# Optimization experiments

Hardware: AMD Instinct MI355X
Metric: run time of the kernel (lower is better)

The kernel has to match this reference:

```python
import jax, jax.numpy as jnp
import numpy as np

HEADS = 4


def setup_inputs() -> dict:
    key = jax.random.key(0)
    kx, kqkv, kbq, ko, kbo = jax.random.split(key, 5)
    B, C, H, W = 4, 256, 64, 64
    x = jax.random.normal(kx, (B, C, H, W), dtype=jnp.float32)
    # torch nn.Linear stores weight as [out_features, in_features]
    w_qkv = jax.random.normal(kqkv, (3 * C, C), dtype=jnp.float32) * (1.0 / np.sqrt(C))
    b_qkv = jax.random.normal(kbq, (3 * C,), dtype=jnp.float32) * 0.02
    w_o = jax.random.normal(ko, (C, C), dtype=jnp.float32) * (1.0 / np.sqrt(C))
    b_o = jax.random.normal(kbo, (C,), dtype=jnp.float32) * 0.02
    return {"x": x, "w_qkv": w_qkv, "b_qkv": b_qkv, "w_o": w_o, "b_o": b_o}


def reference(x, w_qkv, b_qkv, w_o, b_o):
    B, C, H, W = x.shape
    S = H * W
    hd = C // HEADS
    # (B, C, H, W) -> (B, S, C)
    xt = x.reshape(B, C, S).transpose(0, 2, 1)
    qkv = xt @ w_qkv.T + b_qkv                      # (B, S, 3C)
    q, k, v = jnp.split(qkv, 3, axis=-1)
    def to_heads(t):
        return t.reshape(B, S, HEADS, hd).transpose(0, 2, 1, 3)  # (B, h, S, hd)
    q, k, v = to_heads(q), to_heads(k), to_heads(v)
    scores = jnp.einsum('bhqd,bhkd->bhqk', q, k) / jnp.sqrt(jnp.float32(hd))
    attn = jax.nn.softmax(scores, axis=-1)          # dropout inactive (eval)
    out = jnp.einsum('bhqk,bhkd->bhqd', attn, v)    # (B, h, S, hd)
    out = out.transpose(0, 2, 1, 3).reshape(B, S, C)
    y = out @ w_o.T + b_o                            # (B, S, C)
    y = y.reshape(B, H, W, C).transpose(0, 3, 1, 2)  # (B, C, H, W)
    return y
```

## Files before the change

kernel.cpp:

```cpp
#include <hip/hip_runtime.h>
#include <stdint.h>

#define DI __device__ __forceinline__

typedef __attribute__((ext_vector_type(8))) __bf16 bf16x8;
typedef __attribute__((ext_vector_type(8))) unsigned short u16x8;
typedef __attribute__((ext_vector_type(4))) float f32x4;
typedef __attribute__((ext_vector_type(4))) uint32_t u32x4;
typedef __attribute__((ext_vector_type(4))) unsigned short u16x4;
typedef unsigned short u16;

constexpr int Bb = 4, Cc = 256, Ss = 4096, HD = 64;
constexpr int ELEMS = Bb * Cc * Ss;

DI u16 f2bf(float f) {
  union { float f; unsigned u; } x; x.f = f;
  return (u16)((x.u + 0x7FFFu + ((x.u >> 16) & 1u)) >> 16);
}
DI uint32_t pack2bf(float a, float b) {
  union { float f; uint32_t u; } xa, xb;
  xa.f = a; xb.f = b;
  return __builtin_amdgcn_perm(xb.u + 0x8000u, xa.u + 0x8000u, 0x07060302u);
}
DI bf16x8 ldfrag(const u16* p) { return __builtin_bit_cast(bf16x8, *(const u16x8*)p); }

__global__ __launch_bounds__(256) void k_convw(const float* __restrict__ w1, const float* __restrict__ w2,
                                               u16* __restrict__ d1, u16* __restrict__ d2) {
  int i = blockIdx.x * 256 + threadIdx.x;
  if (i < 196608) d1[i] = f2bf(w1[i]);
  if (i < 65536) d2[i] = f2bf(w2[i]);
}

__global__ __launch_bounds__(256) void k_transpose(const float* __restrict__ x, u16* __restrict__ xt) {
  __shared__ u16 T[64][72];
  const int st = blockIdx.x, ct = blockIdx.y, b = blockIdx.z;
  const int tid = threadIdx.x;
#pragma unroll
  for (int e = 0; e < 2; e++) {
    int ss = tid + e * 256;
    int r = ss >> 3, seg = ss & 7;
    size_t base = ((size_t)(b * Cc + ct * 64 + r) << 12) + st * 64 + seg * 8;
    u16x8 t;
#pragma unroll
    for (int j = 0; j < 8; j++) t[j] = f2bf(x[base + j]);
    *(u16x8*)&T[r][seg * 8] = t;
  }
  __syncthreads();
#pragma unroll
  for (int e = 0; e < 2; e++) {
    int ss = tid + e * 256;
    int sr = ss >> 3, cseg = ss & 7;
    u16x8 o;
#pragma unroll
    for (int j = 0; j < 8; j++) o[j] = T[cseg * 8 + j][sr];
    *(u16x8*)(xt + ((size_t)(b * Ss + st * 64 + sr) << 8) + ct * 64 + cseg * 8) = o;
  }
}

DI void stage_tile(const u16* __restrict__ src, int pitch, int r0, int k0, u16 (*dst)[40], int tid) {
#pragma unroll
  for (int e = 0; e < 2; e++) {
    int c = tid + e * 256;
    int row = c >> 2, seg = c & 3;
    u16x8 t = *(const u16x8*)(src + (size_t)(r0 + row) * pitch + k0 + seg * 8);
    *(u16x8*)&dst[row][seg * 8] = t;
  }
}

__global__ __launch_bounds__(256) void k_qkv(const u16* __restrict__ xt, const u16* __restrict__ w,
                                             const float* __restrict__ bias,
                                             u16* __restrict__ q, u16* __restrict__ kk_, u16* __restrict__ vt_) {
  __shared__ u16 As[128][40], Bs[128][40];
  const int tid = threadIdx.x;
  const int wv = tid >> 6, lane = tid & 63;
  const int wm = wv >> 1, wn = wv & 1;
  const int lr = lane & 15, quad = lane >> 4;
  const int r0 = blockIdx.x * 128;
  const int j0 = blockIdx.y * 128;
  f32x4 acc[4][4] = {};
  for (int k0 = 0; k0 < 256; k0 += 32) {
    __syncthreads();
    stage_tile(xt, 256, r0, k0, As, tid);
    stage_tile(w, 256, j0, k0, Bs, tid);
    __syncthreads();
    bf16x8 a[4], b[4];
#pragma unroll
    for (int mt = 0; mt < 4; mt++) a[mt] = ldfrag(&As[wm * 64 + mt * 16 + lr][quad * 8]);
#pragma unroll
    for (int nt = 0; nt < 4; nt++) b[nt] = ldfrag(&Bs[wn * 64 + nt * 16 + lr][quad * 8]);
#pragma unroll
    for (int mt = 0; mt < 4; mt++)
#pragma unroll
      for (int nt = 0; nt < 4; nt++)
        acc[mt][nt] = __builtin_amdgcn_mfma_f32_16x16x32_bf16(a[mt], b[nt], acc[mt][nt], 0, 0, 0);
  }
#pragma unroll
  for (int nt = 0; nt < 4; nt++) {
    int j = j0 + wn * 64 + nt * 16 + lr;
    float bj = bias[j];
    int part = j >> 8, cc = j & 255, head = cc >> 6, d = cc & 63;
#pragma unroll
    for (int mt = 0; mt < 4; mt++)
#pragma unroll
      for (int rg = 0; rg < 4; rg++) {
        int row = r0 + wm * 64 + mt * 16 + quad * 4 + rg;
        int b_ = row >> 12, s = row & 4095;
        float val = acc[mt][nt][rg] + bj;
        if (part == 0) {
          q[((size_t)((b_ * 4 + head) * Ss + s) << 6) + d] = f2bf(val * 0.18033688f);
        } else if (part == 1) {
          kk_[((size_t)((b_ * 4 + head) * Ss + s) << 6) + d] = f2bf(val);
        } else {
          int chunk = s >> 6, w6 = s & 63;
          int t = w6 >> 4, qq = (w6 >> 2) & 3, r = w6 & 3;
          int slot = ((t >> 1) << 5) | (qq << 3) | ((t & 1) << 2) | r;
          vt_[((size_t)((b_ * 4 + head) * 64 + d) << 12) + chunk * 64 + slot] = f2bf(val);
        }
      }
  }
}

__global__ __launch_bounds__(256, 2) void k_attn(const u16* __restrict__ Q, const u16* __restrict__ K,
                                                 const u16* __restrict__ VT, u16* __restrict__ AO,
                                                 float* __restrict__ Opart, float* __restrict__ lpart,
                                                 int nsplit) {
  __shared__ u16 Kl[2][64][72];
  __shared__ u16 Vl[2][64][72];
  const int tid = threadIdx.x;
  const int wv = tid >> 6, lane = tid & 63;
  const int lr = lane & 15, quad = lane >> 4;
  const int bh = blockIdx.y;
  const int b_ = bh >> 2, head = bh & 3;
  const int qbase = blockIdx.x * 256 + wv * 64;
  const int sp = blockIdx.z;
  const int nchunk = 64 / nsplit, kcg0 = sp * nchunk;
  const u16* Qh = Q + (size_t)bh * Ss * HD;
  const u16* Kh = K + (size_t)bh * Ss * HD;
  const u16* Vh = VT + (size_t)bh * HD * Ss;

  bf16x8 qb[4][2];
#pragma unroll
  for (int nt = 0; nt < 4; nt++)
#pragma unroll
    for (int ks = 0; ks < 2; ks++)
      qb[nt][ks] = ldfrag(Qh + (size_t)(qbase + nt * 16 + lr) * HD + ks * 32 + quad * 8);

  f32x4 O[4][4] = {};
  float lsum[4] = {0.f, 0.f, 0.f, 0.f};

  u16x8 pf[4];
  const int srow = tid >> 3, sseg = tid & 7;
  auto load_chunk = [&](int kc) {
#pragma unroll
    for (int e = 0; e < 2; e++) {
      pf[e] = *(const u16x8*)(Kh + ((size_t)((kcg0 + kc) * 64 + srow + e * 32) << 6) + sseg * 8);
      pf[2 + e] = *(const u16x8*)(Vh + ((size_t)(srow + e * 32) << 12) + (kcg0 + kc) * 64 + sseg * 8);
    }
  };
  auto store_chunk = [&](int buf) {
#pragma unroll
    for (int e = 0; e < 2; e++) {
      *(u16x8*)&Kl[buf][srow + e * 32][sseg * 8] = pf[e];
      *(u16x8*)&Vl[buf][srow + e * 32][sseg * 8] = pf[2 + e];
    }
  };

  load_chunk(0);
  store_chunk(0);
  if (nchunk > 1) load_chunk(1);
  __syncthreads();

  for (int kc = 0; kc < nchunk; kc++) {
    const int cur = kc & 1;
    f32x4 St[4][4] = {};
#pragma unroll
    for (int ks = 0; ks < 2; ks++) {
      bf16x8 ka[4];
#pragma unroll
      for (int kt = 0; kt < 4; kt++) ka[kt] = ldfrag(&Kl[cur][kt * 16 + lr][ks * 32 + quad * 8]);
#pragma unroll
      for (int kt = 0; kt < 4; kt++)
#pragma unroll
        for (int nt = 0; nt < 4; nt++)
          St[kt][nt] = __builtin_amdgcn_mfma_f32_16x16x32_bf16(ka[kt], qb[nt][ks], St[kt][nt], 0, 0, 0);
    }

    uint32_t pk[4][4][2];
#pragma unroll
    for (int kt = 0; kt < 4; kt++)
#pragma unroll
      for (int nt = 0; nt < 4; nt++) {
        float p0 = __builtin_amdgcn_exp2f(St[kt][nt][0]);
        float p1 = __builtin_amdgcn_exp2f(St[kt][nt][1]);
        float p2 = __builtin_amdgcn_exp2f(St[kt][nt][2]);
        float p3 = __builtin_amdgcn_exp2f(St[kt][nt][3]);
        lsum[nt] += (p0 + p1) + (p2 + p3);
        pk[kt][nt][0] = pack2bf(p0, p1);
        pk[kt][nt][1] = pack2bf(p2, p3);
      }

#pragma unroll
    for (int ks = 0; ks < 2; ks++) {
      bf16x8 pa[4];
#pragma unroll
      for (int mt = 0; mt < 4; mt++) {
        u32x4 t = {pk[2 * ks][mt][0], pk[2 * ks][mt][1], pk[2 * ks + 1][mt][0], pk[2 * ks + 1][mt][1]};
        pa[mt] = __builtin_bit_cast(bf16x8, t);
      }
#pragma unroll
      for (int dt = 0; dt < 4; dt++) {
        bf16x8 vb = ldfrag(&Vl[cur][dt * 16 + lr][ks * 32 + quad * 8]);
#pragma unroll
        for (int mt = 0; mt < 4; mt++)
          O[mt][dt] = __builtin_amdgcn_mfma_f32_16x16x32_bf16(pa[mt], vb, O[mt][dt], 0, 0, 0);
      }
    }

    if (kc + 1 < nchunk) {
      store_chunk(cur ^ 1);
      if (kc + 2 < nchunk) load_chunk(kc + 2);
    }
    __syncthreads();
  }

#pragma unroll
  for (int nt = 0; nt < 4; nt++) {
    lsum[nt] += __shfl_xor(lsum[nt], 16);
    lsum[nt] += __shfl_xor(lsum[nt], 32);
  }

  if (nsplit == 1) {
#pragma unroll
    for (int mt = 0; mt < 4; mt++)
#pragma unroll
      for (int rg = 0; rg < 4; rg++) {
        float lv = __shfl(lsum[mt], quad * 4 + rg + (lane & 48));
        lv = __shfl(lsum[mt], quad * 4 + rg);
        float inv = 1.0f / lv;
        int s = qbase + mt * 16 + quad * 4 + rg;
#pragma unroll
        for (int dt = 0; dt < 4; dt++)
          AO[((size_t)(b_ * Ss + s) << 8) + head * 64 + dt * 16 + lr] = f2bf(O[mt][dt][rg] * inv);
      }
  } else {
    float* Op = Opart + (size_t)sp * ELEMS;
    float* lp = lpart + (size_t)sp * (16 * Ss) + bh * Ss;
    if (quad == 0) {
#pragma unroll
      for (int nt = 0; nt < 4; nt++) lp[qbase + nt * 16 + lr] = lsum[nt];
    }
#pragma unroll
    for (int mt = 0; mt < 4; mt++)
#pragma unroll
      for (int rg = 0; rg < 4; rg++) {
        int s = qbase + mt * 16 + quad * 4 + rg;
#pragma unroll
        for (int dt = 0; dt < 4; dt++)
          Op[((size_t)(b_ * Ss + s) << 8) + head * 64 + dt * 16 + lr] = O[mt][dt][rg];
      }
  }
}

__global__ __launch_bounds__(256) void k_comb(const float* __restrict__ Opart, const float* __restrict__ lpart,
                                              u16* __restrict__ ao) {
  int idx = (blockIdx.x * 256 + threadIdx.x) * 4;
  f32x4 o0 = *(const f32x4*)(Opart + idx);
  f32x4 o1 = *(const f32x4*)(Opart + (size_t)ELEMS + idx);
  int c = idx & 255, bs = idx >> 8;
  int b = bs >> 12, s = bs & 4095, head = c >> 6;
  int li = (b * 4 + head) * Ss + s;
  float l = lpart[li] + lpart[16 * Ss + li];
  float inv = 1.0f / l;
  u16x4 o;
#pragma unroll
  for (int j = 0; j < 4; j++) o[j] = f2bf((o0[j] + o1[j]) * inv);
  *(u16x4*)(ao + idx) = o;
}

__global__ __launch_bounds__(256) void k_oproj(const u16* __restrict__ wo, const u16* __restrict__ ao,
                                               const float* __restrict__ bo, float* __restrict__ y) {
  __shared__ u16 As[128][40], Bs[128][40];
  const int tid = threadIdx.x;
  const int wv = tid >> 6, lane = tid & 63;
  const int wm = wv >> 1, wn = wv & 1;
  const int lr = lane & 15, quad = lane >> 4;
  const int c0 = blockIdx.x * 128;
  const int n0 = blockIdx.y * 128;
  f32x4 acc[4][4] = {};
  for (int k0 = 0; k0 < 256; k0 += 32) {
    __syncthreads();
    stage_tile(wo, 256, c0, k0, As, tid);
    stage_tile(ao, 256, n0, k0, Bs, tid);
    __syncthreads();
    bf16x8 a[4], b[4];
#pragma unroll
    for (int mt = 0; mt < 4; mt++) a[mt] = ldfrag(&As[wm * 64 + mt * 16 + lr][quad * 8]);
#pragma unroll
    for (int nt = 0; nt < 4; nt++) b[nt] = ldfrag(&Bs[wn * 64 + nt * 16 + lr][quad * 8]);
#pragma unroll
    for (int mt = 0; mt < 4; mt++)
#pragma unroll
      for (int nt = 0; nt < 4; nt++)
        acc[mt][nt] = __builtin_amdgcn_mfma_f32_16x16x32_bf16(a[mt], b[nt], acc[mt][nt], 0, 0, 0);
  }
#pragma unroll
  for (int mt = 0; mt < 4; mt++)
#pragma unroll
    for (int rg = 0; rg < 4; rg++) {
      int c = c0 + wm * 64 + mt * 16 + quad * 4 + rg;
      float bc = bo[c];
#pragma unroll
      for (int nt = 0; nt < 4; nt++) {
        int col = n0 + wn * 64 + nt * 16 + lr;
        int b_ = col >> 12, s = col & 4095;
        y[((size_t)(b_ * Cc + c) << 12) + s] = acc[mt][nt][rg] + bc;
      }
    }
}

extern "C" void kernel_launch(void* const* d_in, const int* in_sizes, int n_in,
                              void* d_out, int out_size, void* d_ws, size_t ws_size,
                              hipStream_t stream) {
  const float* x = (const float*)d_in[0];
  const float* w_qkv = (const float*)d_in[1];
  const float* b_qkv = (const float*)d_in[2];
  const float* w_o = (const float*)d_in[3];
  const float* b_o = (const float*)d_in[4];
  float* y = (float*)d_out;
  u16* ws = (u16*)d_ws;
  u16* xt = ws;
  u16* q = ws + (size_t)ELEMS;
  u16* k = ws + (size_t)2 * ELEMS;
  u16* vt = ws + (size_t)3 * ELEMS;
  u16* ao = xt;
  u16* wqb = ws + (size_t)4 * ELEMS;
  u16* wob = wqb + 196608;
  float* Opart = (float*)(wob + 65536);
  float* lpart = Opart + (size_t)2 * ELEMS;
  const size_t need = ((size_t)4 * ELEMS + 262144) * 2 + (size_t)2 * ELEMS * 4 + (size_t)2 * 16 * Ss * 4;
  const int nsplit = (ws_size >= need) ? 2 : 1;

  k_convw<<<768, 256, 0, stream>>>(w_qkv, w_o, wqb, wob);
  k_transpose<<<dim3(64, 4, 4), 256, 0, stream>>>(x, xt);
  k_qkv<<<dim3(128, 6), 256, 0, stream>>>(xt, wqb, b_qkv, q, k, vt);
  k_attn<<<dim3(16, 16, nsplit), 256, 0, stream>>>(q, k, vt, ao, Opart, lpart, nsplit);
  if (nsplit == 2) k_comb<<<ELEMS / 1024, 256, 0, stream>>>(Opart, lpart, ao);
  k_oproj<<<dim3(2, 128), 256, 0, stream>>>(wob, ao, b_o, y);
}
```

Measured before the change: 190.6 us.

## Split V transpose into its own kernel and allow four-way KV split

```diff
diff --git a/kernel.cpp b/kernel.cpp
--- a/kernel.cpp
+++ b/kernel.cpp
@@ -69,7 +69,7 @@
 
 __global__ __launch_bounds__(256) void k_qkv(const u16* __restrict__ xt, const u16* __restrict__ w,
                                              const float* __restrict__ bias,
-                                             u16* __restrict__ q, u16* __restrict__ kk_, u16* __restrict__ vt_) {
+                                             u16* __restrict__ q, u16* __restrict__ kk_, u16* __restrict__ vv_) {
   __shared__ u16 As[128][40], Bs[128][40];
   const int tid = threadIdx.x;
   const int wv = tid >> 6, lane = tid & 63;
@@ -99,24 +99,42 @@
     int j = j0 + wn * 64 + nt * 16 + lr;
     float bj = bias[j];
     int part = j >> 8, cc = j & 255, head = cc >> 6, d = cc & 63;
+    u16* outp = (part == 0) ? q : (part == 1) ? kk_ : vv_;
+    float sc = (part == 0) ? 0.18033688f : 1.0f;
 #pragma unroll
     for (int mt = 0; mt < 4; mt++)
 #pragma unroll
       for (int rg = 0; rg < 4; rg++) {
         int row = r0 + wm * 64 + mt * 16 + quad * 4 + rg;
         int b_ = row >> 12, s = row & 4095;
-        float val = acc[mt][nt][rg] + bj;
-        if (part == 0) {
-          q[((size_t)((b_ * 4 + head) * Ss + s) << 6) + d] = f2bf(val * 0.18033688f);
-        } else if (part == 1) {
-          kk_[((size_t)((b_ * 4 + head) * Ss + s) << 6) + d] = f2bf(val);
-        } else {
-          int chunk = s >> 6, w6 = s & 63;
-          int t = w6 >> 4, qq = (w6 >> 2) & 3, r = w6 & 3;
-          int slot = ((t >> 1) << 5) | (qq << 3) | ((t & 1) << 2) | r;
-          vt_[((size_t)((b_ * 4 + head) * 64 + d) << 12) + chunk * 64 + slot] = f2bf(val);
-        }
-      }
+        outp[((size_t)((b_ * 4 + head) * Ss + s) << 6) + d] = f2bf((acc[mt][nt][rg] + bj) * sc);
+      }
+  }
+}
+
+__global__ __launch_bounds__(256) void k_vt(const u16* __restrict__ v, u16* __restrict__ vt) {
+  __shared__ u16 T[64][72];
+  const int chunk = blockIdx.x, bh = blockIdx.y;
+  const int tid = threadIdx.x;
+#pragma unroll
+  for (int e = 0; e < 2; e++) {
+    int row = (tid >> 3) + e * 32, seg = tid & 7;
+    *(u16x8*)&T[row][seg * 8] =
+        *(const u16x8*)(v + ((size_t)(bh * Ss + chunk * 64 + row) << 6) + seg * 8);
+  }
+  __syncthreads();
+#pragma unroll
+  for (int e = 0; e < 2; e++) {
+    int d = (tid >> 3) + e * 32, seg = tid & 7;
+    u16x8 o;
+#pragma unroll
+    for (int j = 0; j < 8; j++) {
+      int slot = seg * 8 + j;
+      int t = (((slot >> 5) & 1) << 1) | ((slot >> 2) & 1);
+      int w6 = t * 16 + (((slot >> 3) & 3) << 2) + (slot & 3);
+      o[j] = T[w6][d];
+    }
+    *(u16x8*)(vt + ((size_t)(bh * 64 + d) << 12) + chunk * 64 + seg * 8) = o;
   }
 }
 
@@ -234,8 +252,7 @@
     for (int mt = 0; mt < 4; mt++)
 #pragma unroll
       for (int rg = 0; rg < 4; rg++) {
-        float lv = __shfl(lsum[mt], quad * 4 + rg + (lane & 48));
-        lv = __shfl(lsum[mt], quad * 4 + rg);
+        float lv = __shfl(lsum[mt], quad * 4 + rg);
         float inv = 1.0f / lv;
         int s = qbase + mt * 16 + quad * 4 + rg;
 #pragma unroll
@@ -262,18 +279,23 @@
 }
 
 __global__ __launch_bounds__(256) void k_comb(const float* __restrict__ Opart, const float* __restrict__ lpart,
-                                              u16* __restrict__ ao) {
+                                              u16* __restrict__ ao, int nsplit) {
   int idx = (blockIdx.x * 256 + threadIdx.x) * 4;
-  f32x4 o0 = *(const f32x4*)(Opart + idx);
-  f32x4 o1 = *(const f32x4*)(Opart + (size_t)ELEMS + idx);
   int c = idx & 255, bs = idx >> 8;
   int b = bs >> 12, s = bs & 4095, head = c >> 6;
   int li = (b * 4 + head) * Ss + s;
-  float l = lpart[li] + lpart[16 * Ss + li];
+  f32x4 oacc = *(const f32x4*)(Opart + idx);
+  float l = lpart[li];
+  for (int j = 1; j < nsplit; j++) {
+    f32x4 oj = *(const f32x4*)(Opart + (size_t)j * ELEMS + idx);
+#pragma unroll
+    for (int t = 0; t < 4; t++) oacc[t] += oj[t];
+    l += lpart[(size_t)j * 16 * Ss + li];
+  }
   float inv = 1.0f / l;
   u16x4 o;
 #pragma unroll
-  for (int j = 0; j < 4; j++) o[j] = f2bf((o0[j] + o1[j]) * inv);
+  for (int j = 0; j < 4; j++) o[j] = f2bf(oacc[j] * inv);
   *(u16x4*)(ao + idx) = o;
 }
 
@@ -335,15 +357,19 @@
   u16* ao = xt;
   u16* wqb = ws + (size_t)4 * ELEMS;
   u16* wob = wqb + 196608;
-  float* Opart = (float*)(wob + 65536);
-  float* lpart = Opart + (size_t)2 * ELEMS;
-  const size_t need = ((size_t)4 * ELEMS + 262144) * 2 + (size_t)2 * ELEMS * 4 + (size_t)2 * 16 * Ss * 4;
-  const int nsplit = (ws_size >= need) ? 2 : 1;
+  const size_t Wu16 = (size_t)4 * ELEMS + 262144;
+  float* Opart = (float*)(ws + Wu16);
+  u16* v = (u16*)Opart;
+  const size_t base = Wu16 * 2;
+  auto need = [&](int n) { return base + (size_t)n * ELEMS * 4 + (size_t)n * 16 * Ss * 4; };
+  const int nsplit = (ws_size >= need(4)) ? 4 : (ws_size >= need(2)) ? 2 : 1;
+  float* lpart = Opart + (size_t)nsplit * ELEMS;
 
   k_convw<<<768, 256, 0, stream>>>(w_qkv, w_o, wqb, wob);
   k_transpose<<<dim3(64, 4, 4), 256, 0, stream>>>(x, xt);
-  k_qkv<<<dim3(128, 6), 256, 0, stream>>>(xt, wqb, b_qkv, q, k, vt);
+  k_qkv<<<dim3(128, 6), 256, 0, stream>>>(xt, wqb, b_qkv, q, k, v);
+  k_vt<<<dim3(64, 16), 256, 0, stream>>>(v, vt);
   k_attn<<<dim3(16, 16, nsplit), 256, 0, stream>>>(q, k, vt, ao, Opart, lpart, nsplit);
-  if (nsplit == 2) k_comb<<<ELEMS / 1024, 256, 0, stream>>>(Opart, lpart, ao);
+  if (nsplit > 1) k_comb<<<ELEMS / 1024, 256, 0, stream>>>(Opart, lpart, ao, nsplit);
   k_oproj<<<dim3(2, 128), 256, 0, stream>>>(wob, ao, b_o, y);
 }
```

Result: slower. 198.3 us (+4.0%).
